# Kernel tuning notes

Hardware: AMD Instinct MI355X
Metric: run time of the kernel (lower is better)

Reference implementation:

```python
import jax, jax.numpy as jnp
import numpy as np
import math

# ---- irreps config: (multiplicity, l); parity implied by the fixed path list ----
IRREPS_IN = [(32, 0), (32, 1)]    # "32x0e + 32x1o" -> dim 128
IRREPS_SH = [(1, 0), (1, 1), (1, 2)]  # "1x0e + 1x1o + 1x2e" -> dim 9
IRREPS_OUT = [(32, 0), (32, 1)]   # dim 128
# parity/triangle-allowed 'uvw' instructions: (in_block, sh_block, out_block)
PATHS = [(0, 0, 0), (0, 1, 1), (1, 0, 1), (1, 1, 0), (1, 2, 1)]
NUM_NODES = 50000
NUM_EDGES = 800000


def _fact(n):
    return math.factorial(int(round(n)))


def _su2_cg(j1, j2, j3):
    """SU(2) Clebsch-Gordan coefficients via the Racah formula."""
    C = np.zeros((2 * j1 + 1, 2 * j2 + 1, 2 * j3 + 1))
    for m1 in range(-j1, j1 + 1):
        for m2 in range(-j2, j2 + 1):
            m3 = m1 + m2
            if abs(m3) > j3:
                continue
            vmin = int(max(-j1 + j2 + m3, -j1 + m1, 0))
            vmax = int(min(j2 + j3 + m1, j3 - j1 + j2, j3 + m3))
            c = math.sqrt((2 * j3 + 1) * _fact(j3 + j1 - j2) * _fact(j3 - j1 + j2)
                          * _fact(j1 + j2 - j3) / _fact(j1 + j2 + j3 + 1))
            c *= math.sqrt(_fact(j3 + m3) * _fact(j3 - m3) * _fact(j1 - m1)
                           * _fact(j1 + m1) * _fact(j2 - m2) * _fact(j2 + m2))
            s = 0.0
            for v in range(vmin, vmax + 1):
                s += ((-1.0) ** (v + j2 + m2) * _fact(j2 + j3 + m1 - v) * _fact(j1 - m1 + v)
                      / (_fact(v) * _fact(j3 - j1 + j2 - v) * _fact(j3 + m3 - v) * _fact(v + j1 - j2 - m3)))
            C[j1 + m1, j2 + m2, j3 + m3] = c * s
    return C


def _q(l):
    """Change of basis real -> complex spherical harmonics (e3nn convention)."""
    q = np.zeros((2 * l + 1, 2 * l + 1), dtype=np.complex128)
    for m in range(-l, 0):
        q[l + m, l + abs(m)] = 1.0 / np.sqrt(2.0)
        q[l + m, l - abs(m)] = -1j / np.sqrt(2.0)
    q[l, l] = 1.0
    for m in range(1, l + 1):
        q[l + m, l + abs(m)] = (-1.0) ** m / np.sqrt(2.0)
        q[l + m, l - abs(m)] = 1j * (-1.0) ** m / np.sqrt(2.0)
    return (-1j) ** l * q


def _real_cg(l1, l2, l3):
    """Real (Wigner-3j-like) Clebsch-Gordan tensor, unit Frobenius norm."""
    C = _su2_cg(l1, l2, l3).astype(np.complex128)
    C = np.einsum('ij,kl,mn,ikn->jlm', _q(l1), _q(l2), np.conj(_q(l3).T), C)
    C = np.real(C)
    return (C / np.linalg.norm(C)).astype(np.float32)


CG = [jnp.asarray(_real_cg(IRREPS_IN[i1][1], IRREPS_SH[i2][1], IRREPS_OUT[io][1]))
      for (i1, i2, io) in PATHS]
N_PATHS_TO_OUT = {io: sum(1 for p in PATHS if p[2] == io) for io in range(len(IRREPS_OUT))}


def _split(x, irreps):
    """Split flat irreps vector into [E, mul, 2l+1] blocks."""
    blocks, off = [], 0
    for mul, l in irreps:
        d = mul * (2 * l + 1)
        blocks.append(x[:, off:off + d].reshape(x.shape[0], mul, 2 * l + 1))
        off += d
    return blocks


def setup_inputs() -> dict:
    key = jax.random.key(0)
    k1, k2, k3, k4 = jax.random.split(key, 4)
    in_dim = sum(m * (2 * l + 1) for m, l in IRREPS_IN)
    sh_dim = sum(m * (2 * l + 1) for m, l in IRREPS_SH)
    features = jax.random.normal(k1, (NUM_NODES, in_dim), dtype=jnp.float32)
    edge_sh = jax.random.normal(k2, (NUM_EDGES, sh_dim), dtype=jnp.float32)
    edge_index = jax.random.randint(k3, (2, NUM_EDGES), 0, NUM_NODES, dtype=jnp.int32)
    # shared 'uvw' weights: one [mul_in=32, mul_out=32] matrix per path (mul_sh=1)
    weights = jax.random.normal(k4, (len(PATHS), 32, 32), dtype=jnp.float32)
    return {"features": features, "edge_sh": edge_sh,
            "edge_index": edge_index, "weights": weights}


def reference(features, edge_sh, edge_index, weights):
    src, dst = edge_index[0], edge_index[1]
    x1 = _split(features[src], IRREPS_IN)   # gather source node features per edge
    x2 = _split(edge_sh, IRREPS_SH)
    out_blocks = [None] * len(IRREPS_OUT)
    for p, (i1, i2, io) in enumerate(PATHS):
        u, v = IRREPS_IN[i1][0], IRREPS_SH[i2][0]
        alpha = 1.0 / math.sqrt(u * v * N_PATHS_TO_OUT[io])
        # tmp: [E, u, 2*l3+1]; sh block has mul 1 -> squeeze
        tmp = jnp.einsum('eui,ej,ijk->euk', x1[i1], x2[i2][:, 0, :], CG[p])
        msg = jnp.einsum('euk,uw->ewk', tmp, weights[p]) * alpha
        out_blocks[io] = msg if out_blocks[io] is None else out_blocks[io] + msg
    E = edge_sh.shape[0]
    msgs = jnp.concatenate([b.reshape(E, -1) for b in out_blocks], axis=1)  # [E, 128]
    out = jnp.zeros((features.shape[0], msgs.shape[1]), dtype=features.dtype)
    return out.at[dst].add(msgs)  # scatter-add to destination nodes
```

## Files before the change

### kernel.cpp

```cpp
#include <hip/hip_runtime.h>
#include <math.h>


typedef __attribute__((ext_vector_type(8))) short bf16x8;
typedef __attribute__((ext_vector_type(4))) float f32x4;

__device__ inline float blo(unsigned u) { return __uint_as_float(u << 16); }
__device__ inline float bhi(unsigned u) { return __uint_as_float(u & 0xffff0000u); }
__device__ inline unsigned bpack(float a, float b) {
    unsigned ua = __float_as_uint(a);
    ua = (ua + 0x7fffu + ((ua >> 16) & 1u)) >> 16;
    unsigned ub = __float_as_uint(b);
    ub = (ub + 0x7fffu + ((ub >> 16) & 1u)) & 0xffff0000u;
    return ua | ub;
}
__device__ inline unsigned short bh(float a) {
    unsigned ua = __float_as_uint(a);
    return (unsigned short)((ua + 0x7fffu + ((ua >> 16) & 1u)) >> 16);
}

__device__ inline float dfactf(int n) {
    float r = 1.0f;
    for (int i = 2; i <= n; ++i) r *= (float)i;
    return r;
}

__device__ float su2_cg_elem_f(int l1, int l2, int l3, int i, int k, int n) {
    int m1 = i - l1, m2 = k - l2, m3 = n - l3;
    if (m1 + m2 != m3) return 0.0f;
    int vmin = -l1 + l2 + m3;
    if (-l1 + m1 > vmin) vmin = -l1 + m1;
    if (0 > vmin) vmin = 0;
    int vmax = l2 + l3 + m1;
    if (l3 - l1 + l2 < vmax) vmax = l3 - l1 + l2;
    if (l3 + m3 < vmax) vmax = l3 + m3;
    if (vmax < vmin) return 0.0f;
    float c = sqrtf((float)(2 * l3 + 1) * dfactf(l3 + l1 - l2) *
                    dfactf(l3 - l1 + l2) * dfactf(l1 + l2 - l3) /
                    dfactf(l1 + l2 + l3 + 1));
    c *= sqrtf(dfactf(l3 + m3) * dfactf(l3 - m3) * dfactf(l1 - m1) *
               dfactf(l1 + m1) * dfactf(l2 - m2) * dfactf(l2 + m2));
    float s = 0.0f;
    for (int v = vmin; v <= vmax; ++v) {
        float term = dfactf(l2 + l3 + m1 - v) * dfactf(l1 - m1 + v) /
                     (dfactf(v) * dfactf(l3 - l1 + l2 - v) *
                      dfactf(l3 + m3 - v) * dfactf(v + l1 - l2 - m3));
        if ((v + l2 + m2) & 1) term = -term;
        s += term;
    }
    return c * s;
}

__device__ void cg_compute_block(float* __restrict__ cg_out) {
    __shared__ float sqr[3][5][5], sqi[3][5][5];
    __shared__ float vals[5][45];
    int t = threadIdx.x;
    if (t < 75) {
        int l = t / 25, a = (t % 25) / 5, b = t % 5;
        float re = 0.f, im = 0.f;
        const float inv = 0.70710678118654752440f;
        int m = a - l;
        if (a < 5 && b < 5) {
            if (m < 0) {
                if (b == l - m) re = inv;
                if (b == l + m) im = -inv;
            } else if (m == 0) {
                if (b == l && a == l) re = 1.f;
            } else {
                float sgn = (m & 1) ? -1.f : 1.f;
                if (b == l + m) re = sgn * inv;
                if (b == l - m) im = sgn * inv;
            }
        }
        if (l == 1) { float r = re; re = im; im = -r; }
        else if (l == 2) { re = -re; im = -im; }
        sqr[l][a][b] = re;
        sqi[l][a][b] = im;
    }
    __syncthreads();
    const int l1s[5] = {0, 0, 1, 1, 1};
    const int l2s[5] = {0, 1, 0, 1, 2};
    const int l3s[5] = {0, 1, 1, 0, 1};
    const int offs[5] = {0, 1, 10, 19, 28};
    const float alphas[5] = {0.125f, 0.10206207261596575f, 0.10206207261596575f,
                             0.125f, 0.10206207261596575f};
    int p = t / 45, idx = t % 45;
    bool active = (t < 225);
    float acc = 0.0f;
    int d1 = 0, d2 = 0, d3 = 0;
    if (active) {
        int l1 = l1s[p], l2 = l2s[p], l3 = l3s[p];
        d1 = 2 * l1 + 1; d2 = 2 * l2 + 1; d3 = 2 * l3 + 1;
        if (idx < d1 * d2 * d3) {
            int j = idx / (d2 * d3);
            int rem = idx % (d2 * d3);
            int l_ = rem / d3, m = rem % d3;
            for (int i = 0; i < d1; ++i)
                for (int k = 0; k < d2; ++k)
                    for (int n = 0; n < d3; ++n) {
                        float C = su2_cg_elem_f(l1, l2, l3, i, k, n);
                        if (C == 0.0f) continue;
                        float ar = sqr[l1][i][j], ai = sqi[l1][i][j];
                        float br = sqr[l2][k][l_], bi = sqi[l2][k][l_];
                        float cr = sqr[l3][n][m], ci = sqi[l3][n][m];
                        float abr = ar * br - ai * bi;
                        float abi = ar * bi + ai * br;
                        acc += (abr * cr + abi * ci) * C;
                    }
        }
        vals[p][idx] = acc;
    }
    __syncthreads();
    if (active && idx < d1 * d2 * d3) {
        float n2 = 0.0f;
        for (int q = 0; q < 45; ++q) n2 += vals[p][q] * vals[p][q];
        cg_out[offs[p] + idx] = acc * alphas[p] / sqrtf(n2);
    }
}

__global__ __launch_bounds__(256) void prep_kernel(
    const float* __restrict__ feat, const int* __restrict__ eidx,
    int* __restrict__ cursor, unsigned* __restrict__ fb,
    float* __restrict__ cg, int N, int E) {
    if (blockIdx.x == 0) cg_compute_block(cg);
    int t = blockIdx.x * 256 + threadIdx.x;
    if (t < N * 32) {
        int n = t >> 5, u = t & 31;
        const float* f = feat + (size_t)n * 128;
        float s = f[u];
        float vx = f[32 + 3 * u], vy = f[33 + 3 * u], vz = f[34 + 3 * u];
        ((uint2*)fb)[t] = make_uint2(bpack(s, vx), bpack(vy, vz));
    }
    if (t < E) atomicAdd(&cursor[eidx[E + t]], 1);
}

__global__ __launch_bounds__(256) void scanA_kernel(
    const int* __restrict__ counts, int* __restrict__ tilesums, int N,
    const float* __restrict__ W, const float* __restrict__ cg,
    unsigned short* __restrict__ WBT) {
    __shared__ int lds[4];
    int i = blockIdx.x * 256 + threadIdx.x;
    int v = (i < N) ? counts[i] : 0;
#pragma unroll
    for (int d = 1; d < 64; d <<= 1) v += __shfl_xor(v, d);
    int wid = threadIdx.x >> 6;
    if ((threadIdx.x & 63) == 0) lds[wid] = v;
    __syncthreads();
    if (threadIdx.x == 0)
        tilesums[blockIdx.x] = lds[0] + lds[1] + lds[2] + lds[3];
    int idx = i;
    if (idx < 128 * 352) {
        int j = idx / 352, k = idx % 352;
        int t = k >> 5, u = k & 31;
        float val = 0.f;
        if (j < 32) {
            if (t == 0) val = cg[0] * W[u * 32 + j];
            else if (t == 1) val = W[3072 + u * 32 + j];
        } else {
            int w = (j - 32) / 3, m = (j - 32) % 3;
            if (t >= 2 && t <= 4) { if (t - 2 == m) val = W[1024 + u * 32 + w]; }
            else if (t >= 5 && t <= 7) { val = cg[10 + (t - 5) * 3 + m] * W[2048 + u * 32 + w]; }
            else if (t >= 8) { if (t - 8 == m) val = W[4096 + u * 32 + w]; }
        }
        WBT[idx] = bh(val);
    }
}

__global__ __launch_bounds__(256) void scanB_kernel(
    int* __restrict__ tilesums, int tiles) {
    __shared__ int lds[4];
    int tid = threadIdx.x;
    int v = (tid < tiles) ? tilesums[tid] : 0;
    int orig = v;
#pragma unroll
    for (int d = 1; d < 64; d <<= 1) {
        int t = __shfl_up(v, d);
        if ((tid & 63) >= d) v += t;
    }
    int wid = tid >> 6;
    if ((tid & 63) == 63) lds[wid] = v;
    __syncthreads();
    int base = 0;
    for (int q = 0; q < wid; ++q) base += lds[q];
    if (tid < tiles) tilesums[tid] = base + v - orig;
}

__global__ __launch_bounds__(256) void scanC_kernel(
    int* __restrict__ counts, const int* __restrict__ tilesums, int N) {
    __shared__ int lds[4];
    int i = blockIdx.x * 256 + threadIdx.x;
    int tid = threadIdx.x;
    int v = (i < N) ? counts[i] : 0;
    int orig = v;
#pragma unroll
    for (int d = 1; d < 64; d <<= 1) {
        int t = __shfl_up(v, d);
        if ((tid & 63) >= d) v += t;
    }
    int wid = tid >> 6;
    if ((tid & 63) == 63) lds[wid] = v;
    __syncthreads();
    int base = tilesums[blockIdx.x];
    for (int q = 0; q < wid; ++q) base += lds[q];
    if (i < N) counts[i] = base + v - orig;
}

__global__ __launch_bounds__(256) void zscatter_kernel(
    const int* __restrict__ eidx, const float* __restrict__ sh,
    const float* __restrict__ cg, int* __restrict__ cursor,
    unsigned* __restrict__ zrec, int E) {
    int t = blockIdx.x * 256 + threadIdx.x;
    if (t >= E) return;
    int src = eidx[t];
    int dst = eidx[E + t];
    int pos = atomicAdd(&cursor[dst], 1);
    const float* Ye = sh + (size_t)t * 9;
    float Y0 = Ye[0];
    float Y1v[3] = {Ye[1], Ye[2], Ye[3]};
    float Y2v[5] = {Ye[4], Ye[5], Ye[6], Ye[7], Ye[8]};
    float Z1[3], Z3[3], Z4[9];
#pragma unroll
    for (int m = 0; m < 3; ++m)
        Z1[m] = fmaf(Y1v[0], cg[1 + m],
                fmaf(Y1v[1], cg[4 + m], Y1v[2] * cg[7 + m]));
#pragma unroll
    for (int i = 0; i < 3; ++i)
        Z3[i] = fmaf(Y1v[0], cg[19 + i * 3],
                fmaf(Y1v[1], cg[19 + i * 3 + 1], Y1v[2] * cg[19 + i * 3 + 2]));
#pragma unroll
    for (int i = 0; i < 3; ++i)
#pragma unroll
        for (int m = 0; m < 3; ++m) {
            float acc = 0.f;
#pragma unroll
            for (int j = 0; j < 5; ++j)
                acc = fmaf(Y2v[j], cg[28 + (i * 5 + j) * 3 + m], acc);
            Z4[i * 3 + m] = acc;
        }
    uint2* rec = (uint2*)(zrec + (size_t)pos * 10);
    rec[0] = make_uint2((unsigned)src, bpack(Y0, Z1[0]));
    rec[1] = make_uint2(bpack(Z1[1], Z1[2]), bpack(Z3[0], Z3[1]));
    rec[2] = make_uint2(bpack(Z3[2], Z4[0]), bpack(Z4[1], Z4[2]));
    rec[3] = make_uint2(bpack(Z4[3], Z4[4]), bpack(Z4[5], Z4[6]));
    rec[4] = make_uint2(bpack(Z4[7], Z4[8]), 0u);
}

__global__ __launch_bounds__(256) void gather_mfma_kernel(
    const unsigned* __restrict__ fb, const unsigned* __restrict__ zrec,
    const int* __restrict__ cursor, const unsigned short* __restrict__ WBT,
    float* __restrict__ out, int N) {
    __shared__ unsigned short Gs[16][360];
    int wv = threadIdx.x >> 6;
    int lane = threadIdx.x & 63;
    int half = lane >> 5, u = lane & 31;
    int base = blockIdx.x << 4;

#pragma unroll 1
    for (int d = 0; d < 4; ++d) {
        int row = wv * 4 + d;
        int node = base + row;
        if (node >= N) break;
        int start = node ? cursor[node - 1] : 0;
        int end = cursor[node];

        float g0 = 0.f, g3 = 0.f;
        float g1x = 0.f, g1y = 0.f, g1z = 0.f;
        float g2x = 0.f, g2y = 0.f, g2z = 0.f;
        float g4x = 0.f, g4y = 0.f, g4z = 0.f;

        for (int idx = start + half; idx < end; idx += 2) {
            const uint2* r = (const uint2*)(zrec + (size_t)idx * 10);
            uint2 r0 = r[0], r1 = r[1], r2 = r[2], r3 = r[3], r4 = r[4];
            int src = (int)r0.x;
            uint2 f2 = ((const uint2*)fb)[(size_t)src * 32 + u];
            float s = blo(f2.x), vx = bhi(f2.x);
            float vy = blo(f2.y), vz = bhi(f2.y);
            float y0 = blo(r0.y), z10 = bhi(r0.y);
            float z11 = blo(r1.x), z12 = bhi(r1.x);
            float z30 = blo(r1.y), z31 = bhi(r1.y);
            float z32 = blo(r2.x), z400 = bhi(r2.x);
            float z401 = blo(r2.y), z402 = bhi(r2.y);
            float z410 = blo(r3.x), z411 = bhi(r3.x);
            float z412 = blo(r3.y), z420 = bhi(r3.y);
            float z421 = blo(r4.x), z422 = bhi(r4.x);

            g0 = fmaf(y0, s, g0);
            g1x = fmaf(z10, s, g1x); g1y = fmaf(z11, s, g1y); g1z = fmaf(z12, s, g1z);
            g2x = fmaf(y0, vx, g2x); g2y = fmaf(y0, vy, g2y); g2z = fmaf(y0, vz, g2z);
            g3 = fmaf(z30, vx, fmaf(z31, vy, fmaf(z32, vz, g3)));
            g4x = fmaf(vx, z400, fmaf(vy, z410, fmaf(vz, z420, g4x)));
            g4y = fmaf(vx, z401, fmaf(vy, z411, fmaf(vz, z421, g4y)));
            g4z = fmaf(vx, z402, fmaf(vy, z412, fmaf(vz, z422, g4z)));
        }
        g0 += __shfl_xor(g0, 32);  g3 += __shfl_xor(g3, 32);
        g1x += __shfl_xor(g1x, 32); g1y += __shfl_xor(g1y, 32); g1z += __shfl_xor(g1z, 32);
        g2x += __shfl_xor(g2x, 32); g2y += __shfl_xor(g2y, 32); g2z += __shfl_xor(g2z, 32);
        g4x += __shfl_xor(g4x, 32); g4y += __shfl_xor(g4y, 32); g4z += __shfl_xor(g4z, 32);

        if (half == 0) {
            unsigned short* Gr = &Gs[row][u];
            Gr[0] = bh(g0);
            Gr[32] = bh(g3);
            Gr[64] = bh(g1x);  Gr[96] = bh(g1y);  Gr[128] = bh(g1z);
            Gr[160] = bh(g2x); Gr[192] = bh(g2y); Gr[224] = bh(g2z);
            Gr[256] = bh(g4x); Gr[288] = bh(g4y); Gr[320] = bh(g4z);
        }
    }
    __syncthreads();

    int r = lane & 15, q = lane >> 4;
    bf16x8 a[11];
#pragma unroll
    for (int kk = 0; kk < 11; ++kk)
        a[kk] = *(const bf16x8*)(&Gs[r][kk * 32 + q * 8]);

#pragma unroll
    for (int jj = 0; jj < 2; ++jj) {
        int jt = wv * 2 + jj;
        f32x4 acc = {0.f, 0.f, 0.f, 0.f};
#pragma unroll
        for (int kk = 0; kk < 11; ++kk) {
            bf16x8 b = *(const bf16x8*)(WBT + (size_t)(jt * 16 + r) * 352 + kk * 32 + q * 8);
            acc = __builtin_amdgcn_mfma_f32_16x16x32_bf16(a[kk], b, acc, 0, 0, 0);
        }
#pragma unroll
        for (int i = 0; i < 4; ++i) {
            int n = base + q * 4 + i;
            if (n < N) out[(size_t)n * 128 + jt * 16 + r] = acc[i];
        }
    }
}

extern "C" void kernel_launch(void* const* d_in, const int* in_sizes, int n_in,
                              void* d_out, int out_size, void* d_ws, size_t ws_size,
                              hipStream_t stream) {
    const float* feat = (const float*)d_in[0];
    const float* sh = (const float*)d_in[1];
    const int* eidx = (const int*)d_in[2];
    const float* W = (const float*)d_in[3];
    float* out = (float*)d_out;
    int N = in_sizes[0] / 128;
    int E = in_sizes[1] / 9;

    float* wsf = (float*)d_ws;
    float* cg = wsf;
    int* cursor = (int*)(wsf + 128);
    size_t off = (size_t)(128 + N + 1) & ~(size_t)1;
    unsigned* zrec = (unsigned*)(wsf + off);
    unsigned* fb = zrec + (size_t)10 * E;
    unsigned short* WBT = (unsigned short*)(fb + (size_t)64 * N);
    int* tilesums = (int*)(WBT + 45056);

    int tiles = (N + 255) / 256;
    int ntiles16 = (N + 15) / 16;

    hipMemsetAsync(cursor, 0, (size_t)N * sizeof(int), stream);
    prep_kernel<<<(N * 32 + 255) / 256, 256, 0, stream>>>(feat, eidx, cursor, fb, cg, N, E);
    scanA_kernel<<<tiles, 256, 0, stream>>>(cursor, tilesums, N, W, cg, WBT);
    scanB_kernel<<<1, 256, 0, stream>>>(tilesums, tiles);
    scanC_kernel<<<tiles, 256, 0, stream>>>(cursor, tilesums, N);
    zscatter_kernel<<<(E + 255) / 256, 256, 0, stream>>>(eidx, sh, cg, cursor, zrec, E);
    gather_mfma_kernel<<<ntiles16, 256, 0, stream>>>(fb, zrec, cursor, WBT, out, N);
}
```

Before: 179.5 us.

## Scatter only edge ids and compute per-edge CG records in the gather kernel's LDS

The scatter pass now writes only the edge id into a destination-sorted order array instead of a 40-byte packed record per edge. The gather kernel, now 512 threads per 16-node tile, stages each chunk of edges cooperatively: it reads the edge id, src and SH, computes the CG-contracted Z values into shared memory, and then the waves accumulate from LDS. This removes a large intermediate write and reread through global memory. In exchange it adds random reads of sh and eidx in the gather, extra barriers and LDS use, and one MFMA output tile per wave instead of two.

```diff
diff --git a/kernel.cpp b/kernel.cpp
--- a/kernel.cpp
+++ b/kernel.cpp
@@ -205,105 +205,132 @@
     if (i < N) counts[i] = base + v - orig;
 }
 
-__global__ __launch_bounds__(256) void zscatter_kernel(
-    const int* __restrict__ eidx, const float* __restrict__ sh,
-    const float* __restrict__ cg, int* __restrict__ cursor,
-    unsigned* __restrict__ zrec, int E) {
+__global__ __launch_bounds__(256) void scatter_ids_kernel(
+    const int* __restrict__ eidx, int* __restrict__ cursor,
+    int* __restrict__ eorder, int E) {
     int t = blockIdx.x * 256 + threadIdx.x;
     if (t >= E) return;
-    int src = eidx[t];
-    int dst = eidx[E + t];
-    int pos = atomicAdd(&cursor[dst], 1);
-    const float* Ye = sh + (size_t)t * 9;
-    float Y0 = Ye[0];
-    float Y1v[3] = {Ye[1], Ye[2], Ye[3]};
-    float Y2v[5] = {Ye[4], Ye[5], Ye[6], Ye[7], Ye[8]};
-    float Z1[3], Z3[3], Z4[9];
-#pragma unroll
-    for (int m = 0; m < 3; ++m)
-        Z1[m] = fmaf(Y1v[0], cg[1 + m],
-                fmaf(Y1v[1], cg[4 + m], Y1v[2] * cg[7 + m]));
-#pragma unroll
-    for (int i = 0; i < 3; ++i)
-        Z3[i] = fmaf(Y1v[0], cg[19 + i * 3],
-                fmaf(Y1v[1], cg[19 + i * 3 + 1], Y1v[2] * cg[19 + i * 3 + 2]));
-#pragma unroll
-    for (int i = 0; i < 3; ++i)
-#pragma unroll
-        for (int m = 0; m < 3; ++m) {
-            float acc = 0.f;
-#pragma unroll
-            for (int j = 0; j < 5; ++j)
-                acc = fmaf(Y2v[j], cg[28 + (i * 5 + j) * 3 + m], acc);
-            Z4[i * 3 + m] = acc;
-        }
-    uint2* rec = (uint2*)(zrec + (size_t)pos * 10);
-    rec[0] = make_uint2((unsigned)src, bpack(Y0, Z1[0]));
-    rec[1] = make_uint2(bpack(Z1[1], Z1[2]), bpack(Z3[0], Z3[1]));
-    rec[2] = make_uint2(bpack(Z3[2], Z4[0]), bpack(Z4[1], Z4[2]));
-    rec[3] = make_uint2(bpack(Z4[3], Z4[4]), bpack(Z4[5], Z4[6]));
-    rec[4] = make_uint2(bpack(Z4[7], Z4[8]), 0u);
-}
-
-__global__ __launch_bounds__(256) void gather_mfma_kernel(
-    const unsigned* __restrict__ fb, const unsigned* __restrict__ zrec,
+    int pos = atomicAdd(&cursor[eidx[E + t]], 1);
+    eorder[pos] = t;
+}
+
+__global__ __launch_bounds__(512) void gather_mfma_kernel(
+    const unsigned* __restrict__ fb, const float* __restrict__ sh,
+    const int* __restrict__ eidx, const int* __restrict__ eorder,
     const int* __restrict__ cursor, const unsigned short* __restrict__ WBT,
-    float* __restrict__ out, int N) {
+    const float* __restrict__ cg, float* __restrict__ out, int N) {
+    __shared__ unsigned Zs[512][12];
     __shared__ unsigned short Gs[16][360];
-    int wv = threadIdx.x >> 6;
-    int lane = threadIdx.x & 63;
+    int tid = threadIdx.x;
+    int wv = tid >> 6, lane = tid & 63;
     int half = lane >> 5, u = lane & 31;
     int base = blockIdx.x << 4;
-
-#pragma unroll 1
-    for (int d = 0; d < 4; ++d) {
-        int row = wv * 4 + d;
-        int node = base + row;
-        if (node >= N) break;
-        int start = node ? cursor[node - 1] : 0;
-        int end = cursor[node];
-
-        float g0 = 0.f, g3 = 0.f;
-        float g1x = 0.f, g1y = 0.f, g1z = 0.f;
-        float g2x = 0.f, g2y = 0.f, g2z = 0.f;
-        float g4x = 0.f, g4y = 0.f, g4z = 0.f;
-
-        for (int idx = start + half; idx < end; idx += 2) {
-            const uint2* r = (const uint2*)(zrec + (size_t)idx * 10);
-            uint2 r0 = r[0], r1 = r[1], r2 = r[2], r3 = r[3], r4 = r[4];
-            int src = (int)r0.x;
-            uint2 f2 = ((const uint2*)fb)[(size_t)src * 32 + u];
-            float s = blo(f2.x), vx = bhi(f2.x);
-            float vy = blo(f2.y), vz = bhi(f2.y);
-            float y0 = blo(r0.y), z10 = bhi(r0.y);
-            float z11 = blo(r1.x), z12 = bhi(r1.x);
-            float z30 = blo(r1.y), z31 = bhi(r1.y);
-            float z32 = blo(r2.x), z400 = bhi(r2.x);
-            float z401 = blo(r2.y), z402 = bhi(r2.y);
-            float z410 = blo(r3.x), z411 = bhi(r3.x);
-            float z412 = blo(r3.y), z420 = bhi(r3.y);
-            float z421 = blo(r4.x), z422 = bhi(r4.x);
-
-            g0 = fmaf(y0, s, g0);
-            g1x = fmaf(z10, s, g1x); g1y = fmaf(z11, s, g1y); g1z = fmaf(z12, s, g1z);
-            g2x = fmaf(y0, vx, g2x); g2y = fmaf(y0, vy, g2y); g2z = fmaf(y0, vz, g2z);
-            g3 = fmaf(z30, vx, fmaf(z31, vy, fmaf(z32, vz, g3)));
-            g4x = fmaf(vx, z400, fmaf(vy, z410, fmaf(vz, z420, g4x)));
-            g4y = fmaf(vx, z401, fmaf(vy, z411, fmaf(vz, z421, g4y)));
-            g4z = fmaf(vx, z402, fmaf(vy, z412, fmaf(vz, z422, g4z)));
-        }
-        g0 += __shfl_xor(g0, 32);  g3 += __shfl_xor(g3, 32);
-        g1x += __shfl_xor(g1x, 32); g1y += __shfl_xor(g1y, 32); g1z += __shfl_xor(g1z, 32);
-        g2x += __shfl_xor(g2x, 32); g2y += __shfl_xor(g2y, 32); g2z += __shfl_xor(g2z, 32);
-        g4x += __shfl_xor(g4x, 32); g4y += __shfl_xor(g4y, 32); g4z += __shfl_xor(g4z, 32);
-
+    int lastnode = (base + 15 < N) ? base + 15 : N - 1;
+    int r0 = base ? cursor[base - 1] : 0;
+    int r1 = cursor[lastnode];
+
+    int s0 = 0, e0 = 0, s1 = 0, e1 = 0;
+    {
+        int na = base + wv * 2, nb = na + 1;
+        if (na < N) { s0 = na ? cursor[na - 1] : 0; e0 = cursor[na]; }
+        if (nb < N) { s1 = cursor[nb - 1]; e1 = cursor[nb]; }
+    }
+    float g[2][11];
+#pragma unroll
+    for (int d = 0; d < 2; ++d)
+#pragma unroll
+        for (int k = 0; k < 11; ++k) g[d][k] = 0.f;
+
+    for (int c0 = r0; c0 < r1; c0 += 512) {
+        int c1 = (c0 + 512 < r1) ? c0 + 512 : r1;
+        __syncthreads();
+        if (tid < c1 - c0) {
+            int e = eorder[c0 + tid];
+            int src = eidx[e];
+            const float* Ye = sh + (size_t)e * 9;
+            float Y0 = Ye[0];
+            float Y1v[3] = {Ye[1], Ye[2], Ye[3]};
+            float Y2v[5] = {Ye[4], Ye[5], Ye[6], Ye[7], Ye[8]};
+            float Z1[3], Z3[3], Z4[9];
+#pragma unroll
+            for (int m = 0; m < 3; ++m)
+                Z1[m] = fmaf(Y1v[0], cg[1 + m],
+                        fmaf(Y1v[1], cg[4 + m], Y1v[2] * cg[7 + m]));
+#pragma unroll
+            for (int i = 0; i < 3; ++i)
+                Z3[i] = fmaf(Y1v[0], cg[19 + i * 3],
+                        fmaf(Y1v[1], cg[19 + i * 3 + 1], Y1v[2] * cg[19 + i * 3 + 2]));
+#pragma unroll
+            for (int i = 0; i < 3; ++i)
+#pragma unroll
+                for (int m = 0; m < 3; ++m) {
+                    float acc = 0.f;
+#pragma unroll
+                    for (int j = 0; j < 5; ++j)
+                        acc = fmaf(Y2v[j], cg[28 + (i * 5 + j) * 3 + m], acc);
+                    Z4[i * 3 + m] = acc;
+                }
+            unsigned* Zr = Zs[tid];
+            Zr[0] = (unsigned)src;
+            Zr[2] = bpack(Y0, Z1[0]);
+            Zr[3] = bpack(Z1[1], Z1[2]);
+            Zr[4] = bpack(Z3[0], Z3[1]);
+            Zr[5] = bpack(Z3[2], Z4[0]);
+            Zr[6] = bpack(Z4[1], Z4[2]);
+            Zr[7] = bpack(Z4[3], Z4[4]);
+            Zr[8] = bpack(Z4[5], Z4[6]);
+            Zr[9] = bpack(Z4[7], Z4[8]);
+        }
+        __syncthreads();
+#pragma unroll
+        for (int d = 0; d < 2; ++d) {
+            int s = d ? s1 : s0;
+            int e = d ? e1 : e0;
+            int lo = (s > c0) ? s : c0;
+            int hi = (e < c1) ? e : c1;
+            int first = lo + ((s + half - lo) & 1);
+            for (int idx = first; idx < hi; idx += 2) {
+                const unsigned* Zr = Zs[idx - c0];
+                int src = (int)Zr[0];
+                uint2 z0 = *(const uint2*)(Zr + 2);
+                uint2 z1 = *(const uint2*)(Zr + 4);
+                uint2 z2 = *(const uint2*)(Zr + 6);
+                uint2 z3 = *(const uint2*)(Zr + 8);
+                uint2 f2 = ((const uint2*)fb)[(size_t)src * 32 + u];
+                float sF = blo(f2.x), vx = bhi(f2.x);
+                float vy = blo(f2.y), vz = bhi(f2.y);
+                float y0 = blo(z0.x), z10 = bhi(z0.x);
+                float z11 = blo(z0.y), z12 = bhi(z0.y);
+                float z30 = blo(z1.x), z31 = bhi(z1.x);
+                float z32 = blo(z1.y), z400 = bhi(z1.y);
+                float z401 = blo(z2.x), z402 = bhi(z2.x);
+                float z410 = blo(z2.y), z411 = bhi(z2.y);
+                float z412 = blo(z3.x), z420 = bhi(z3.x);
+                float z421 = blo(z3.y), z422 = bhi(z3.y);
+
+                g[d][0] = fmaf(y0, sF, g[d][0]);
+                g[d][1] = fmaf(z30, vx, fmaf(z31, vy, fmaf(z32, vz, g[d][1])));
+                g[d][2] = fmaf(z10, sF, g[d][2]);
+                g[d][3] = fmaf(z11, sF, g[d][3]);
+                g[d][4] = fmaf(z12, sF, g[d][4]);
+                g[d][5] = fmaf(y0, vx, g[d][5]);
+                g[d][6] = fmaf(y0, vy, g[d][6]);
+                g[d][7] = fmaf(y0, vz, g[d][7]);
+                g[d][8] = fmaf(vx, z400, fmaf(vy, z410, fmaf(vz, z420, g[d][8])));
+                g[d][9] = fmaf(vx, z401, fmaf(vy, z411, fmaf(vz, z421, g[d][9])));
+                g[d][10] = fmaf(vx, z402, fmaf(vy, z412, fmaf(vz, z422, g[d][10])));
+            }
+        }
+    }
+#pragma unroll
+    for (int d = 0; d < 2; ++d) {
+#pragma unroll
+        for (int k = 0; k < 11; ++k) g[d][k] += __shfl_xor(g[d][k], 32);
         if (half == 0) {
+            int row = wv * 2 + d;
             unsigned short* Gr = &Gs[row][u];
-            Gr[0] = bh(g0);
-            Gr[32] = bh(g3);
-            Gr[64] = bh(g1x);  Gr[96] = bh(g1y);  Gr[128] = bh(g1z);
-            Gr[160] = bh(g2x); Gr[192] = bh(g2y); Gr[224] = bh(g2z);
-            Gr[256] = bh(g4x); Gr[288] = bh(g4y); Gr[320] = bh(g4z);
+#pragma unroll
+            for (int k = 0; k < 11; ++k) Gr[k * 32] = bh(g[d][k]);
         }
     }
     __syncthreads();
@@ -313,21 +340,17 @@
 #pragma unroll
     for (int kk = 0; kk < 11; ++kk)
         a[kk] = *(const bf16x8*)(&Gs[r][kk * 32 + q * 8]);
-
-#pragma unroll
-    for (int jj = 0; jj < 2; ++jj) {
-        int jt = wv * 2 + jj;
-        f32x4 acc = {0.f, 0.f, 0.f, 0.f};
-#pragma unroll
-        for (int kk = 0; kk < 11; ++kk) {
-            bf16x8 b = *(const bf16x8*)(WBT + (size_t)(jt * 16 + r) * 352 + kk * 32 + q * 8);
-            acc = __builtin_amdgcn_mfma_f32_16x16x32_bf16(a[kk], b, acc, 0, 0, 0);
-        }
-#pragma unroll
-        for (int i = 0; i < 4; ++i) {
-            int n = base + q * 4 + i;
-            if (n < N) out[(size_t)n * 128 + jt * 16 + r] = acc[i];
-        }
+    int jt = wv;
+    f32x4 acc = {0.f, 0.f, 0.f, 0.f};
+#pragma unroll
+    for (int kk = 0; kk < 11; ++kk) {
+        bf16x8 b = *(const bf16x8*)(WBT + (size_t)(jt * 16 + r) * 352 + kk * 32 + q * 8);
+        acc = __builtin_amdgcn_mfma_f32_16x16x32_bf16(a[kk], b, acc, 0, 0, 0);
+    }
+#pragma unroll
+    for (int i = 0; i < 4; ++i) {
+        int n = base + q * 4 + i;
+        if (n < N) out[(size_t)n * 128 + jt * 16 + r] = acc[i];
     }
 }
 
@@ -345,9 +368,8 @@
     float* wsf = (float*)d_ws;
     float* cg = wsf;
     int* cursor = (int*)(wsf + 128);
-    size_t off = (size_t)(128 + N + 1) & ~(size_t)1;
-    unsigned* zrec = (unsigned*)(wsf + off);
-    unsigned* fb = zrec + (size_t)10 * E;
+    int* eorder = cursor + N;
+    unsigned* fb = (unsigned*)(eorder + E);
     unsigned short* WBT = (unsigned short*)(fb + (size_t)64 * N);
     int* tilesums = (int*)(WBT + 45056);
 
@@ -359,6 +381,6 @@
     scanA_kernel<<<tiles, 256, 0, stream>>>(cursor, tilesums, N, W, cg, WBT);
     scanB_kernel<<<1, 256, 0, stream>>>(tilesums, tiles);
     scanC_kernel<<<tiles, 256, 0, stream>>>(cursor, tilesums, N);
-    zscatter_kernel<<<(E + 255) / 256, 256, 0, stream>>>(eidx, sh, cg, cursor, zrec, E);
-    gather_mfma_kernel<<<ntiles16, 256, 0, stream>>>(fb, zrec, cursor, WBT, out, N);
-}
+    scatter_ids_kernel<<<(E + 255) / 256, 256, 0, stream>>>(eidx, cursor, eorder, E);
+    gather_mfma_kernel<<<ntiles16, 512, 0, stream>>>(fb, sh, eidx, eorder, cursor, WBT, cg, out, N);
+}
```

Result: slower. 196.7 us (+9.6%).

## Fold CG contraction into weight matrix and gather raw SH via edge order

Applied to the files above, without the earlier changes.

Removes the per-edge Z-record precompute and the 40-byte record write. The scatter pass now stores only the edge ID in sorted order. The gather kernel reads the raw 9-float SH and src index indirectly, accumulates 31 outer-product terms per channel, and contracts them against a larger CG-folded weight matrix (K=992) with MFMA. This trades less scatter-pass traffic for more indirect reads, more register accumulators, a larger LDS tile and roughly three times the MFMA work.

```diff
diff --git a/kernel.cpp b/kernel.cpp
--- a/kernel.cpp
+++ b/kernel.cpp
@@ -137,7 +137,7 @@
 __global__ __launch_bounds__(256) void scanA_kernel(
     const int* __restrict__ counts, int* __restrict__ tilesums, int N,
     const float* __restrict__ W, const float* __restrict__ cg,
-    unsigned short* __restrict__ WBT) {
+    unsigned short* __restrict__ WBT, int nthreads) {
     __shared__ int lds[4];
     int i = blockIdx.x * 256 + threadIdx.x;
     int v = (i < N) ? counts[i] : 0;
@@ -148,21 +148,26 @@
     __syncthreads();
     if (threadIdx.x == 0)
         tilesums[blockIdx.x] = lds[0] + lds[1] + lds[2] + lds[3];
-    int idx = i;
-    if (idx < 128 * 352) {
-        int j = idx / 352, k = idx % 352;
+    for (int w = i; w < 128 * 992; w += nthreads) {
+        int j = w / 992, k = w % 992;
         int t = k >> 5, u = k & 31;
         float val = 0.f;
         if (j < 32) {
             if (t == 0) val = cg[0] * W[u * 32 + j];
-            else if (t == 1) val = W[3072 + u * 32 + j];
+            else if (t >= 7 && t < 16) {
+                int r = t - 7, jy = r / 3, ii = r % 3;
+                val = cg[19 + ii * 3 + jy] * W[3072 + u * 32 + j];
+            }
         } else {
-            int w = (j - 32) / 3, m = (j - 32) % 3;
-            if (t >= 2 && t <= 4) { if (t - 2 == m) val = W[1024 + u * 32 + w]; }
-            else if (t >= 5 && t <= 7) { val = cg[10 + (t - 5) * 3 + m] * W[2048 + u * 32 + w]; }
-            else if (t >= 8) { if (t - 8 == m) val = W[4096 + u * 32 + w]; }
-        }
-        WBT[idx] = bh(val);
+            int wch = (j - 32) / 3, m = (j - 32) % 3;
+            if (t >= 1 && t <= 3) val = cg[1 + (t - 1) * 3 + m] * W[1024 + u * 32 + wch];
+            else if (t >= 4 && t <= 6) val = cg[10 + (t - 4) * 3 + m] * W[2048 + u * 32 + wch];
+            else if (t >= 16) {
+                int r = t - 16, jy = r / 3, ii = r % 3;
+                val = cg[28 + (ii * 5 + jy) * 3 + m] * W[4096 + u * 32 + wch];
+            }
+        }
+        WBT[w] = bh(val);
     }
 }
 
@@ -205,55 +210,50 @@
     if (i < N) counts[i] = base + v - orig;
 }
 
-__global__ __launch_bounds__(256) void zscatter_kernel(
-    const int* __restrict__ eidx, const float* __restrict__ sh,
-    const float* __restrict__ cg, int* __restrict__ cursor,
-    unsigned* __restrict__ zrec, int E) {
+__global__ __launch_bounds__(256) void scatter_ids_kernel(
+    const int* __restrict__ eidx, int* __restrict__ cursor,
+    int* __restrict__ eorder, int E) {
     int t = blockIdx.x * 256 + threadIdx.x;
     if (t >= E) return;
-    int src = eidx[t];
-    int dst = eidx[E + t];
-    int pos = atomicAdd(&cursor[dst], 1);
-    const float* Ye = sh + (size_t)t * 9;
-    float Y0 = Ye[0];
-    float Y1v[3] = {Ye[1], Ye[2], Ye[3]};
-    float Y2v[5] = {Ye[4], Ye[5], Ye[6], Ye[7], Ye[8]};
-    float Z1[3], Z3[3], Z4[9];
-#pragma unroll
-    for (int m = 0; m < 3; ++m)
-        Z1[m] = fmaf(Y1v[0], cg[1 + m],
-                fmaf(Y1v[1], cg[4 + m], Y1v[2] * cg[7 + m]));
+    int pos = atomicAdd(&cursor[eidx[E + t]], 1);
+    eorder[pos] = t;
+}
+
+__device__ inline void edge_accum31(const float* __restrict__ Y, uint2 f2,
+                                    float g[31]) {
+    float s = blo(f2.x), vx = bhi(f2.x);
+    float vy = blo(f2.y), vz = bhi(f2.y);
+    float v3[3] = {vx, vy, vz};
+    g[0] = fmaf(Y[0], s, g[0]);
+#pragma unroll
+    for (int jy = 0; jy < 3; ++jy)
+        g[1 + jy] = fmaf(Y[1 + jy], s, g[1 + jy]);
 #pragma unroll
     for (int i = 0; i < 3; ++i)
-        Z3[i] = fmaf(Y1v[0], cg[19 + i * 3],
-                fmaf(Y1v[1], cg[19 + i * 3 + 1], Y1v[2] * cg[19 + i * 3 + 2]));
-#pragma unroll
-    for (int i = 0; i < 3; ++i)
-#pragma unroll
-        for (int m = 0; m < 3; ++m) {
-            float acc = 0.f;
-#pragma unroll
-            for (int j = 0; j < 5; ++j)
-                acc = fmaf(Y2v[j], cg[28 + (i * 5 + j) * 3 + m], acc);
-            Z4[i * 3 + m] = acc;
-        }
-    uint2* rec = (uint2*)(zrec + (size_t)pos * 10);
-    rec[0] = make_uint2((unsigned)src, bpack(Y0, Z1[0]));
-    rec[1] = make_uint2(bpack(Z1[1], Z1[2]), bpack(Z3[0], Z3[1]));
-    rec[2] = make_uint2(bpack(Z3[2], Z4[0]), bpack(Z4[1], Z4[2]));
-    rec[3] = make_uint2(bpack(Z4[3], Z4[4]), bpack(Z4[5], Z4[6]));
-    rec[4] = make_uint2(bpack(Z4[7], Z4[8]), 0u);
+        g[4 + i] = fmaf(Y[0], v3[i], g[4 + i]);
+#pragma unroll
+    for (int jy = 0; jy < 3; ++jy)
+#pragma unroll
+        for (int i = 0; i < 3; ++i)
+            g[7 + jy * 3 + i] = fmaf(Y[1 + jy], v3[i], g[7 + jy * 3 + i]);
+#pragma unroll
+    for (int jy = 0; jy < 5; ++jy)
+#pragma unroll
+        for (int i = 0; i < 3; ++i)
+            g[16 + jy * 3 + i] = fmaf(Y[4 + jy], v3[i], g[16 + jy * 3 + i]);
 }
 
 __global__ __launch_bounds__(256) void gather_mfma_kernel(
-    const unsigned* __restrict__ fb, const unsigned* __restrict__ zrec,
+    const unsigned* __restrict__ fb, const float* __restrict__ sh,
+    const int* __restrict__ eidx, const int* __restrict__ eorder,
     const int* __restrict__ cursor, const unsigned short* __restrict__ WBT,
     float* __restrict__ out, int N) {
-    __shared__ unsigned short Gs[16][360];
+    __shared__ unsigned short Gs[16][1000];
     int wv = threadIdx.x >> 6;
     int lane = threadIdx.x & 63;
     int half = lane >> 5, u = lane & 31;
     int base = blockIdx.x << 4;
+    const uint2* fb2 = (const uint2*)fb;
 
 #pragma unroll 1
     for (int d = 0; d < 4; ++d) {
@@ -263,70 +263,66 @@
         int start = node ? cursor[node - 1] : 0;
         int end = cursor[node];
 
-        float g0 = 0.f, g3 = 0.f;
-        float g1x = 0.f, g1y = 0.f, g1z = 0.f;
-        float g2x = 0.f, g2y = 0.f, g2z = 0.f;
-        float g4x = 0.f, g4y = 0.f, g4z = 0.f;
-
-        for (int idx = start + half; idx < end; idx += 2) {
-            const uint2* r = (const uint2*)(zrec + (size_t)idx * 10);
-            uint2 r0 = r[0], r1 = r[1], r2 = r[2], r3 = r[3], r4 = r[4];
-            int src = (int)r0.x;
-            uint2 f2 = ((const uint2*)fb)[(size_t)src * 32 + u];
-            float s = blo(f2.x), vx = bhi(f2.x);
-            float vy = blo(f2.y), vz = bhi(f2.y);
-            float y0 = blo(r0.y), z10 = bhi(r0.y);
-            float z11 = blo(r1.x), z12 = bhi(r1.x);
-            float z30 = blo(r1.y), z31 = bhi(r1.y);
-            float z32 = blo(r2.x), z400 = bhi(r2.x);
-            float z401 = blo(r2.y), z402 = bhi(r2.y);
-            float z410 = blo(r3.x), z411 = bhi(r3.x);
-            float z412 = blo(r3.y), z420 = bhi(r3.y);
-            float z421 = blo(r4.x), z422 = bhi(r4.x);
-
-            g0 = fmaf(y0, s, g0);
-            g1x = fmaf(z10, s, g1x); g1y = fmaf(z11, s, g1y); g1z = fmaf(z12, s, g1z);
-            g2x = fmaf(y0, vx, g2x); g2y = fmaf(y0, vy, g2y); g2z = fmaf(y0, vz, g2z);
-            g3 = fmaf(z30, vx, fmaf(z31, vy, fmaf(z32, vz, g3)));
-            g4x = fmaf(vx, z400, fmaf(vy, z410, fmaf(vz, z420, g4x)));
-            g4y = fmaf(vx, z401, fmaf(vy, z411, fmaf(vz, z421, g4y)));
-            g4z = fmaf(vx, z402, fmaf(vy, z412, fmaf(vz, z422, g4z)));
-        }
-        g0 += __shfl_xor(g0, 32);  g3 += __shfl_xor(g3, 32);
-        g1x += __shfl_xor(g1x, 32); g1y += __shfl_xor(g1y, 32); g1z += __shfl_xor(g1z, 32);
-        g2x += __shfl_xor(g2x, 32); g2y += __shfl_xor(g2y, 32); g2z += __shfl_xor(g2z, 32);
-        g4x += __shfl_xor(g4x, 32); g4y += __shfl_xor(g4y, 32); g4z += __shfl_xor(g4z, 32);
-
+        float g[31];
+#pragma unroll
+        for (int k = 0; k < 31; ++k) g[k] = 0.f;
+
+        int idx = start + half;
+        for (; idx + 2 < end; idx += 4) {
+            int eA = eorder[idx];
+            int eB = eorder[idx + 2];
+            int srcA = eidx[eA];
+            int srcB = eidx[eB];
+            const float* YA = sh + (size_t)eA * 9;
+            const float* YB = sh + (size_t)eB * 9;
+            float ya[9], yb[9];
+#pragma unroll
+            for (int q = 0; q < 9; ++q) ya[q] = YA[q];
+#pragma unroll
+            for (int q = 0; q < 9; ++q) yb[q] = YB[q];
+            uint2 fA = fb2[(size_t)srcA * 32 + u];
+            uint2 fB = fb2[(size_t)srcB * 32 + u];
+            edge_accum31(ya, fA, g);
+            edge_accum31(yb, fB, g);
+        }
+        if (idx < end) {
+            int e = eorder[idx];
+            int src = eidx[e];
+            const float* Ye = sh + (size_t)e * 9;
+            float y[9];
+#pragma unroll
+            for (int q = 0; q < 9; ++q) y[q] = Ye[q];
+            uint2 f2 = fb2[(size_t)src * 32 + u];
+            edge_accum31(y, f2, g);
+        }
+#pragma unroll
+        for (int k = 0; k < 31; ++k) g[k] += __shfl_xor(g[k], 32);
         if (half == 0) {
             unsigned short* Gr = &Gs[row][u];
-            Gr[0] = bh(g0);
-            Gr[32] = bh(g3);
-            Gr[64] = bh(g1x);  Gr[96] = bh(g1y);  Gr[128] = bh(g1z);
-            Gr[160] = bh(g2x); Gr[192] = bh(g2y); Gr[224] = bh(g2z);
-            Gr[256] = bh(g4x); Gr[288] = bh(g4y); Gr[320] = bh(g4z);
+#pragma unroll
+            for (int k = 0; k < 31; ++k) Gr[k * 32] = bh(g[k]);
         }
     }
     __syncthreads();
 
     int r = lane & 15, q = lane >> 4;
-    bf16x8 a[11];
-#pragma unroll
-    for (int kk = 0; kk < 11; ++kk)
-        a[kk] = *(const bf16x8*)(&Gs[r][kk * 32 + q * 8]);
-
-#pragma unroll
-    for (int jj = 0; jj < 2; ++jj) {
-        int jt = wv * 2 + jj;
-        f32x4 acc = {0.f, 0.f, 0.f, 0.f};
-#pragma unroll
-        for (int kk = 0; kk < 11; ++kk) {
-            bf16x8 b = *(const bf16x8*)(WBT + (size_t)(jt * 16 + r) * 352 + kk * 32 + q * 8);
-            acc = __builtin_amdgcn_mfma_f32_16x16x32_bf16(a[kk], b, acc, 0, 0, 0);
-        }
-#pragma unroll
-        for (int i = 0; i < 4; ++i) {
-            int n = base + q * 4 + i;
-            if (n < N) out[(size_t)n * 128 + jt * 16 + r] = acc[i];
+    int jt0 = wv * 2, jt1 = wv * 2 + 1;
+    f32x4 acc0 = {0.f, 0.f, 0.f, 0.f};
+    f32x4 acc1 = {0.f, 0.f, 0.f, 0.f};
+#pragma unroll
+    for (int kk = 0; kk < 31; ++kk) {
+        bf16x8 a = *(const bf16x8*)(&Gs[r][kk * 32 + q * 8]);
+        bf16x8 b0 = *(const bf16x8*)(WBT + (size_t)(jt0 * 16 + r) * 992 + kk * 32 + q * 8);
+        bf16x8 b1 = *(const bf16x8*)(WBT + (size_t)(jt1 * 16 + r) * 992 + kk * 32 + q * 8);
+        acc0 = __builtin_amdgcn_mfma_f32_16x16x32_bf16(a, b0, acc0, 0, 0, 0);
+        acc1 = __builtin_amdgcn_mfma_f32_16x16x32_bf16(a, b1, acc1, 0, 0, 0);
+    }
+#pragma unroll
+    for (int i = 0; i < 4; ++i) {
+        int n = base + q * 4 + i;
+        if (n < N) {
+            out[(size_t)n * 128 + jt0 * 16 + r] = acc0[i];
+            out[(size_t)n * 128 + jt1 * 16 + r] = acc1[i];
         }
     }
 }
@@ -345,20 +341,19 @@
     float* wsf = (float*)d_ws;
     float* cg = wsf;
     int* cursor = (int*)(wsf + 128);
-    size_t off = (size_t)(128 + N + 1) & ~(size_t)1;
-    unsigned* zrec = (unsigned*)(wsf + off);
-    unsigned* fb = zrec + (size_t)10 * E;
+    int* eorder = cursor + N;
+    unsigned* fb = (unsigned*)(eorder + E);
     unsigned short* WBT = (unsigned short*)(fb + (size_t)64 * N);
-    int* tilesums = (int*)(WBT + 45056);
+    int* tilesums = (int*)(WBT + 128 * 992);
 
     int tiles = (N + 255) / 256;
     int ntiles16 = (N + 15) / 16;
 
     hipMemsetAsync(cursor, 0, (size_t)N * sizeof(int), stream);
     prep_kernel<<<(N * 32 + 255) / 256, 256, 0, stream>>>(feat, eidx, cursor, fb, cg, N, E);
-    scanA_kernel<<<tiles, 256, 0, stream>>>(cursor, tilesums, N, W, cg, WBT);
+    scanA_kernel<<<tiles, 256, 0, stream>>>(cursor, tilesums, N, W, cg, WBT, tiles * 256);
     scanB_kernel<<<1, 256, 0, stream>>>(tilesums, tiles);
     scanC_kernel<<<tiles, 256, 0, stream>>>(cursor, tilesums, N);
-    zscatter_kernel<<<(E + 255) / 256, 256, 0, stream>>>(eidx, sh, cg, cursor, zrec, E);
-    gather_mfma_kernel<<<ntiles16, 256, 0, stream>>>(fb, zrec, cursor, WBT, out, N);
-}
+    scatter_ids_kernel<<<(E + 255) / 256, 256, 0, stream>>>(eidx, cursor, eorder, E);
+    gather_mfma_kernel<<<ntiles16, 256, 0, stream>>>(fb, sh, eidx, eorder, cursor, WBT, out, N);
+}
```

After: 247.6 us. 37.9% more time.
